# Kernel tuning notes

Measured on AMD Instinct MI355X. Metric: run time of the kernel, lower is better.

The kernel has to match this reference:

```python
import jax, jax.numpy as jnp
import numpy as np

H, W = 72, 128            # raster_h, raster_w
THICK = 0.03              # raster_thickness
SHARP = 80.0              # sigmoid sharpness
RESAMPLE_N = 96           # resample count used for geometric matching costs
PTS_W, TAN_W, CURV_W, OVL_W = 5.0, 1.0, 0.5, 2.0


def _safe_norm(x, axis=-1):
    # faithful to torch.norm; tiny floor only to keep sqrt grad finite
    return jnp.sqrt(jnp.maximum((x * x).sum(axis), 1e-12))


def _grid_xy(h, w):
    ys = jnp.linspace(0.0, 1.0, h)
    xs = jnp.linspace(0.0, 1.0, w)
    yy, xx = jnp.meshgrid(ys, xs, indexing='ij')
    return jnp.stack([xx, yy], axis=-1).reshape(-1, 2)  # [H*W, 2]


def _prepare_mask(vis):
    # mirrors _batched_prepare_curves: fallback to all-ones when <2 visible pts
    raw = vis > 0.5
    fallback = raw.sum(-1) < 2
    return jnp.where(fallback[:, None], 1.0, raw.astype(vis.dtype))  # [m,p]


def _soft_mask(points, point_mask, grid):
    # points [m,p,2], grid [HW,2] -> sigmoid distance field [m, HW]
    seg_a = points[:, :-1]
    ab = points[:, 1:] - seg_a                              # [m,S,2]
    denom = jnp.maximum((ab * ab).sum(-1), 1e-8)            # [m,S]
    seg_valid = (point_mask[:, :-1] * point_mask[:, 1:]) > 0.5
    pts = grid[None, :, None, :]                            # [1,HW,1,2]
    ap = pts - seg_a[:, None]                               # [m,HW,S,2]
    t = jnp.clip((ap * ab[:, None]).sum(-1) / denom[:, None], 0.0, 1.0)
    proj = seg_a[:, None] + t[..., None] * ab[:, None]      # [m,HW,S,2]
    dist = _safe_norm(pts - proj)                           # [m,HW,S]
    dist = jnp.where(seg_valid[:, None, :], dist, jnp.inf)
    min_dist = dist.min(-1)                                 # [m,HW]
    # fallback: curves with no valid segment use nearest visible point
    pdist = _safe_norm(grid[None, :, None, :] - points[:, None])  # [m,HW,p]
    pdist = jnp.where(point_mask[:, None, :] > 0.5, pdist, jnp.inf)
    no_seg = ~seg_valid.any(-1)
    min_dist = jnp.where(no_seg[:, None], pdist.min(-1), min_dist)
    return jax.nn.sigmoid((THICK - min_dist) * SHARP)       # [m,HW]


def _resample(points, point_mask, num):
    # arclength resampling, mirrors _batched_resample_polyline
    m, p, _ = points.shape
    seg_valid = point_mask[:, :-1] * point_mask[:, 1:]
    seg_len = _safe_norm(points[:, 1:] - points[:, :-1]) * seg_valid  # [m,p-1]
    cum = jnp.concatenate([jnp.zeros((m, 1), points.dtype),
                           jnp.cumsum(seg_len, -1)], axis=-1)          # [m,p]
    total = cum[:, -1]
    base_t = jnp.linspace(0.0, 1.0, num)
    t = base_t[None, :] * total[:, None]                               # [m,num]
    idx = jax.vmap(lambda c, tt: jnp.searchsorted(c, tt, side='right'))(cum, t) - 1
    idx = jnp.clip(idx, 0, p - 2)
    left = jnp.take_along_axis(points[:, :-1], idx[..., None], axis=1)
    right = jnp.take_along_axis(points[:, 1:], idx[..., None], axis=1)
    lt = jnp.take_along_axis(cum[:, :-1], idx, axis=1)
    rt = jnp.take_along_axis(cum[:, 1:], idx, axis=1)
    alpha = ((t - lt) / jnp.maximum(rt - lt, 1e-8))[..., None]
    out = left + alpha * (right - left)
    return jnp.where((total < 1e-8)[:, None, None], points[:, :1, :], out)


def _pt2poly(A, B):
    # A [qa,r,2] sample points; B [qb,r,2] polylines -> mean min dist [qa,qb]
    seg_a = B[:, :-1]
    ab = B[:, 1:] - seg_a                                   # [qb,S,2]
    denom = jnp.maximum((ab * ab).sum(-1), 1e-8)            # [qb,S]
    pts = A[:, None, :, None, :]                            # [qa,1,r,1,2]
    ap = pts - seg_a[None, :, None]                         # [qa,qb,r,S,2]
    t = jnp.clip((ap * ab[None, :, None]).sum(-1) / denom[None, :, None], 0.0, 1.0)
    proj = seg_a[None, :, None] + t[..., None] * ab[None, :, None]
    dist = _safe_norm(pts - proj)                           # [qa,qb,r,S]
    return dist.min(-1).mean(-1)                            # [qa,qb]


def _tangents(pts):
    # central differences, endpoints one-sided, unit-normalized
    fwd = jnp.concatenate([pts[:, 1:2] - pts[:, 0:1],
                           pts[:, 2:] - pts[:, :-2],
                           pts[:, -1:] - pts[:, -2:-1]], axis=1)
    n = jnp.maximum(jnp.sqrt((fwd * fwd).sum(-1, keepdims=True)), 1e-8)
    return fwd / n


def _smooth_l1(x):
    a = jnp.abs(x)
    return jnp.where(a < 1.0, 0.5 * a * a, a - 0.5)


def lane_match_cost(pred_pts, gt_pts, gt_vis):
    grid = _grid_xy(H, W)
    m_pred = jnp.ones(pred_pts.shape[:2], pred_pts.dtype)
    m_gt = _prepare_mask(gt_vis)
    # geometric pairwise costs on resampled curves
    pred_rs = _resample(pred_pts, m_pred, RESAMPLE_N)       # [Q,r,2]
    gt_rs = _resample(gt_pts, m_gt, RESAMPLE_N)             # [G,r,2]
    sym = 0.5 * (_pt2poly(pred_rs, gt_rs) + _pt2poly(gt_rs, pred_rs).T)
    pt = _tangents(pred_rs)
    gt_t = _tangents(gt_rs)
    tan = 1.0 - jnp.abs((pt[:, None] * gt_t[None]).sum(-1)).mean(-1)
    ps = pred_rs[:, 2:] - 2 * pred_rs[:, 1:-1] + pred_rs[:, :-2]
    gs = gt_rs[:, 2:] - 2 * gt_rs[:, 1:-1] + gt_rs[:, :-2]
    curv = _smooth_l1(ps[:, None] - gs[None]).mean((-1, -2))
    # soft raster overlap (1 - soft IoU)
    pm = _soft_mask(pred_pts, m_pred, grid)                 # [Q,HW]
    gm = _soft_mask(gt_pts, m_gt, grid)                     # [G,HW]
    inter = pm @ gm.T
    union = pm.sum(-1)[:, None] + gm.sum(-1)[None, :] - inter
    overlap = 1.0 - inter / jnp.maximum(union, 1e-8)
    return PTS_W * sym + TAN_W * tan + CURV_W * curv + OVL_W * overlap


def setup_inputs() -> dict:
    key = jax.random.key(0)
    k1, k2, k3 = jax.random.split(key, 3)
    Q, G, P = 100, 50, 24
    pred_pts = jax.random.uniform(k1, (Q, P, 2), dtype=jnp.float32)
    gt_pts = jax.random.uniform(k2, (G, P, 2), dtype=jnp.float32)
    gt_vis = jax.random.uniform(k3, (G, P), dtype=jnp.float32)
    return {"pred_pts": pred_pts, "gt_pts": gt_pts, "gt_vis": gt_vis}


def reference(pred_pts, gt_pts, gt_vis):
    return lane_match_cost(pred_pts, gt_pts, gt_vis)  # [Q,G] match cost
```

## Files before the change

### kernel.cpp

```cpp
#include <hip/hip_runtime.h>
#include <hip/hip_bf16.h>
#include <math.h>

#define Q_N 100
#define G_N 50
#define P_N 24
#define RS_N 96
#define GRID_N 9216
#define THICK 0.03f
#define SHARP 80.0f
#define PTS_W 5.0f
#define TAN_W 1.0f
#define CURV_W 0.5f
#define OVL_W 2.0f

#define PRS_OFF  0
#define GRS_OFF  19200
#define PMB_OFF  28800
#define GMB_OFF  544896
#define ROWP_OFF 839808
#define ROWG_OFF 840708
#define INTP_OFF 841216

typedef float    f32x2 __attribute__((ext_vector_type(2)));
typedef float    f32x4 __attribute__((ext_vector_type(4)));
typedef _Float16 f16x8 __attribute__((ext_vector_type(8)));

__device__ __forceinline__ float smooth_l1(float x) {
    float a = fabsf(x);
    return (a < 1.0f) ? 0.5f * a * a : a - 0.5f;
}
__device__ __forceinline__ float fast_rcp(float x) {
#if __has_builtin(__builtin_amdgcn_rcpf)
    return __builtin_amdgcn_rcpf(x);
#else
    return 1.0f / x;
#endif
}
__device__ __forceinline__ float fast_sqrt(float x) {
#if __has_builtin(__builtin_amdgcn_sqrtf)
    return __builtin_amdgcn_sqrtf(x);
#else
    return sqrtf(x);
#endif
}

__global__ __launch_bounds__(256)
void mask_kernel(const float* __restrict__ pred,
                 const float* __restrict__ gt,
                 const float* __restrict__ vis,
                 float* __restrict__ ws) {
    int row   = blockIdx.x / 9;
    int chunk = blockIdx.x % 9;
    int tid = threadIdx.x;
    bool isPred = row < Q_N;
    __shared__ float ptx[P_N], pty[P_N], pvv[P_N];
    __shared__ float4 seg[P_N-1];
    __shared__ float  sinv[P_N-1];
    __shared__ int s_noseg;
    __shared__ float wsum[4];
    __shared__ float cum[P_N];
    __shared__ float s_total;

    if (tid < P_N) {
        const float* src = isPred ? pred + row * (P_N*2) : gt + (row - Q_N) * (P_N*2);
        float2 p = ((const float2*)src)[tid];
        ptx[tid] = p.x; pty[tid] = p.y;
    }
    if (tid == 0) {
        s_noseg = 1;
        if (isPred) {
            for (int k = 0; k < P_N; k++) pvv[k] = 1.0f;
        } else {
            const float* v = vis + (row - Q_N) * P_N;
            int cnt = 0;
            for (int k = 0; k < P_N; k++) {
                int r = (v[k] > 0.5f) ? 1 : 0;
                cnt += r;
                pvv[k] = (float)r;
            }
            if (cnt < 2) for (int k = 0; k < P_N; k++) pvv[k] = 1.0f;
        }
    }
    __syncthreads();
    if (tid < P_N-1) {
        bool v = pvv[tid] * pvv[tid+1] > 0.5f;
        if (v) {
            float ax = ptx[tid], ay = pty[tid];
            float abx = ptx[tid+1]-ax, aby = pty[tid+1]-ay;
            seg[tid] = make_float4(ax, ay, abx, aby);
            sinv[tid] = fast_rcp(fmaxf(abx*abx + aby*aby, 1e-8f));
            s_noseg = 0;
        } else {
            seg[tid] = make_float4(1e18f, 1e18f, 0.0f, 0.0f);
            sinv[tid] = 0.0f;
        }
    }
    __syncthreads();

    int g0 = chunk * 1024 + tid * 4;
    float y  = (float)(g0 >> 7) * (1.0f/71.0f);
    float x0 = (float)(g0 & 127) * (1.0f/127.0f);
    f32x2 xs01 = { x0,                  x0 + 1.0f/127.0f };
    f32x2 xs23 = { x0 + 2.0f/127.0f,    x0 + 3.0f/127.0f };
    f32x2 m01 = {3.0e38f, 3.0e38f}, m23 = {3.0e38f, 3.0e38f};
    #pragma unroll
    for (int k = 0; k < P_N-1; k++) {
        float4 sg = seg[k];
        float inv = sinv[k];
        float apy = y - sg.y;
        float dwy = apy * sg.w;
        f32x2 apx01 = xs01 - sg.x;
        f32x2 apx23 = xs23 - sg.x;
        f32x2 t01 = (apx01*sg.z + dwy) * inv;
        f32x2 t23 = (apx23*sg.z + dwy) * inv;
        t01.x = fminf(fmaxf(t01.x, 0.0f), 1.0f);
        t01.y = fminf(fmaxf(t01.y, 0.0f), 1.0f);
        t23.x = fminf(fmaxf(t23.x, 0.0f), 1.0f);
        t23.y = fminf(fmaxf(t23.y, 0.0f), 1.0f);
        f32x2 dx01 = apx01 - t01*sg.z;
        f32x2 dy01 = apy   - t01*sg.w;
        f32x2 dx23 = apx23 - t23*sg.z;
        f32x2 dy23 = apy   - t23*sg.w;
        f32x2 d01 = dx01*dx01 + dy01*dy01;
        f32x2 d23 = dx23*dx23 + dy23*dy23;
        m01.x = fminf(m01.x, d01.x); m01.y = fminf(m01.y, d01.y);
        m23.x = fminf(m23.x, d23.x); m23.y = fminf(m23.y, d23.y);
    }
    float m2[4] = { m01.x, m01.y, m23.x, m23.y };
    if (s_noseg) {
        float xs[4] = { xs01.x, xs01.y, xs23.x, xs23.y };
        #pragma unroll
        for (int u = 0; u < 4; u++) m2[u] = 3.0e38f;
        for (int k = 0; k < P_N; k++) {
            if (pvv[k] > 0.5f) {
                #pragma unroll
                for (int u = 0; u < 4; u++) {
                    float dx = xs[u] - ptx[k], dy = y - pty[k];
                    m2[u] = fminf(m2[u], dx*dx + dy*dy);
                }
            }
        }
    }
    ushort4 o;
    unsigned short* ov = &o.x;
    float lsum = 0.0f;
    #pragma unroll
    for (int u = 0; u < 4; u++) {
        float mind = fast_sqrt(fmaxf(m2[u], 1e-12f));
        float z = (THICK - mind) * SHARP;
        float s = fast_rcp(1.0f + __expf(-z));
        _Float16 h = (_Float16)s;
        ov[u] = __builtin_bit_cast(unsigned short, h);
        lsum += (float)h;
    }
    unsigned short* base = (unsigned short*)(ws + (isPred ? PMB_OFF : GMB_OFF))
                         + (size_t)(isPred ? row : row - Q_N) * GRID_N;
    ((ushort4*)base)[g0 >> 2] = o;

    #pragma unroll
    for (int off = 32; off > 0; off >>= 1) lsum += __shfl_down(lsum, off);
    if ((tid & 63) == 0) wsum[tid >> 6] = lsum;
    __syncthreads();
    if (tid == 0) {
        float s = (wsum[0] + wsum[1]) + (wsum[2] + wsum[3]);
        if (isPred) ws[ROWP_OFF + row*9 + chunk] = s;
        else        ws[ROWG_OFF + (row - Q_N)*9 + chunk] = s;
    }

    if (chunk == 0) {
        if (tid == 0) {
            float c = 0.0f;
            cum[0] = 0.0f;
            for (int k = 0; k < P_N-1; k++) {
                float dx = ptx[k+1]-ptx[k], dy = pty[k+1]-pty[k];
                float len = sqrtf(fmaxf(dx*dx + dy*dy, 1e-12f));
                float valid = pvv[k]*pvv[k+1];
                c += len * valid;
                cum[k+1] = c;
            }
            s_total = c;
        }
        __syncthreads();
        float total = s_total;
        if (tid < RS_N) {
            float ox, oy;
            if (total < 1e-8f) {
                ox = ptx[0]; oy = pty[0];
            } else {
                float t = ((float)tid / 95.0f) * total;
                int idx = -1;
                for (int k = 0; k < P_N; k++) idx += (cum[k] <= t) ? 1 : 0;
                idx = min(max(idx, 0), P_N-2);
                float lt = cum[idx], rt = cum[idx+1];
                float alpha = (t - lt) / fmaxf(rt - lt, 1e-8f);
                ox = ptx[idx] + alpha * (ptx[idx+1]-ptx[idx]);
                oy = pty[idx] + alpha * (pty[idx+1]-pty[idx]);
            }
            float* dst = isPred ? ws + PRS_OFF + row * (RS_N*2)
                                : ws + GRS_OFF + (row - Q_N) * (RS_N*2);
            dst[2*tid]   = ox;
            dst[2*tid+1] = oy;
        }
    }
}

__global__ __launch_bounds__(64)
void inter_kernel(float* __restrict__ ws) {
    int bid = blockIdx.x;
    int mt = bid % 7;
    int nt = (bid / 7) & 3;
    int kc = bid / 28;
    int l = threadIdx.x;
    const unsigned short* PMB = (const unsigned short*)(ws + PMB_OFF);
    const unsigned short* GMB = (const unsigned short*)(ws + GMB_OFF);
    int i0 = mt*16, j0 = nt*16, k0 = kc*1024;
    const f16x8* pa = (const f16x8*)(PMB + (size_t)(i0 + (l & 15)) * GRID_N + k0 + 8*(l >> 4));
    const f16x8* pb = (const f16x8*)(GMB + (size_t)(j0 + (l & 15)) * GRID_N + k0 + 8*(l >> 4));
    f32x4 acc = {0.0f, 0.0f, 0.0f, 0.0f};
    #pragma unroll 8
    for (int s = 0; s < 32; s++) {
        acc = __builtin_amdgcn_mfma_f32_16x16x32_f16(pa[s*4], pb[s*4], acc, 0, 0, 0);
    }
    float* dst = ws + INTP_OFF + kc * 7168;
    int r0 = 4*(l >> 4), c = l & 15;
    #pragma unroll
    for (int v = 0; v < 4; v++) {
        dst[(i0 + r0 + v) * 64 + (j0 + c)] = acc[v];
    }
}

__global__ __launch_bounds__(256)
void pair_kernel(const float* __restrict__ ws, float* __restrict__ out) {
    int bi = blockIdx.x / 25;
    int bj = blockIdx.x % 25;
    int i0 = bi*2, j0 = bj*2;
    int tid = threadIdx.x;
    int w = tid >> 6;
    int l = tid & 63;
    int wi = w >> 1, wj = w & 1;
    int i = i0 + wi, j = j0 + wj;

    __shared__ float Apts[2][RS_N*2], Bpts[2][RS_N*2];
    __shared__ float4 Aseg[2][RS_N-1], Bseg[2][RS_N-1];
    __shared__ float  AInv[2][RS_N-1], BInv[2][RS_N-1];

    float e_ip = 0.0f, e_rp = 0.0f, e_rg = 0.0f;
    if (l < 9) {
        e_ip = ws[INTP_OFF + l*7168 + i*64 + j];
        e_rp = ws[ROWP_OFF + i*9 + l];
        e_rg = ws[ROWG_OFF + j*9 + l];
    }

    if (tid < 192) {
        int side = tid / 96;
        int r = (tid / 48) & 1;
        int o = tid % 48;
        const float4* src = (const float4*)(ws + (side ? GRS_OFF + (j0+r)*(RS_N*2)
                                                       : PRS_OFF + (i0+r)*(RS_N*2)));
        ((float4*)(side ? Bpts[r] : Apts[r]))[o] = src[o];
    }
    __syncthreads();
    for (int q = tid; q < 4*(RS_N-1); q += 256) {
        int side = q / (2*(RS_N-1));
        int rr = (q / (RS_N-1)) & 1;
        int s = q % (RS_N-1);
        const float* P = side ? Bpts[rr] : Apts[rr];
        float ax = P[2*s], ay = P[2*s+1];
        float abx = P[2*s+2]-ax, aby = P[2*s+3]-ay;
        float inv = fast_rcp(fmaxf(abx*abx + aby*aby, 1e-8f));
        if (side) { Bseg[rr][s] = make_float4(ax,ay,abx,aby); BInv[rr][s] = inv; }
        else      { Aseg[rr][s] = make_float4(ax,ay,abx,aby); AInv[rr][s] = inv; }
    }
    __syncthreads();

    bool bSide = l >= 32;
    int h = l & 31;
    const float*  myP = bSide ? Bpts[wj] : Apts[wi];
    const float4* SG  = bSide ? Aseg[wi] : Bseg[wj];
    const float*  SI  = bSide ? AInv[wi] : BInv[wj];
    f32x2 px01 = { myP[6*h+0], myP[6*h+2] };
    f32x2 py01 = { myP[6*h+1], myP[6*h+3] };
    float px2 = myP[6*h+4], py2 = myP[6*h+5];
    f32x2 m01 = {3.0e38f, 3.0e38f};
    float m22 = 3.0e38f;
    #pragma unroll 5
    for (int s = 0; s < RS_N-1; s++) {
        float4 sg = SG[s];
        float inv = SI[s];
        {
            f32x2 apx = px01 - sg.x;
            f32x2 apy = py01 - sg.y;
            f32x2 t = (apx*sg.z + apy*sg.w) * inv;
            t.x = fminf(fmaxf(t.x, 0.0f), 1.0f);
            t.y = fminf(fmaxf(t.y, 0.0f), 1.0f);
            f32x2 dx = apx - t*sg.z;
            f32x2 dy = apy - t*sg.w;
            f32x2 d2 = dx*dx + dy*dy;
            m01.x = fminf(m01.x, d2.x);
            m01.y = fminf(m01.y, d2.y);
        }
        {
            float apx = px2-sg.x, apy = py2-sg.y;
            float t = fminf(fmaxf((apx*sg.z + apy*sg.w)*inv, 0.0f), 1.0f);
            float dx = apx - t*sg.z, dy = apy - t*sg.w;
            m22 = fminf(m22, dx*dx + dy*dy);
        }
    }
    float cham = fast_sqrt(fmaxf(m01.x, 1e-12f)) + fast_sqrt(fmaxf(m01.y, 1e-12f))
               + fast_sqrt(fmaxf(m22, 1e-12f));

    const float* AX = Apts[wi];
    const float* BX = Bpts[wj];
    float tsum = 0.0f, csum = 0.0f;
    #pragma unroll
    for (int rep = 0; rep < 2; rep++) {
        int p = l + rep*64;
        if (p < RS_N) {
            int pl = (p == 0) ? 0 : p-1;
            int pr = (p == RS_N-1) ? RS_N-1 : p+1;
            float tax = AX[2*pr]-AX[2*pl], tay = AX[2*pr+1]-AX[2*pl+1];
            float na = fmaxf(fast_sqrt(tax*tax + tay*tay), 1e-8f);
            float tbx = BX[2*pr]-BX[2*pl], tby = BX[2*pr+1]-BX[2*pl+1];
            float nb = fmaxf(fast_sqrt(tbx*tbx + tby*tby), 1e-8f);
            tsum += fabsf((tax*tbx + tay*tby) * fast_rcp(na*nb));
            if (p < RS_N-2) {
                float psx = AX[2*p+4] - 2.0f*AX[2*p+2] + AX[2*p];
                float psy = AX[2*p+5] - 2.0f*AX[2*p+3] + AX[2*p+1];
                float gsx = BX[2*p+4] - 2.0f*BX[2*p+2] + BX[2*p];
                float gsy = BX[2*p+5] - 2.0f*BX[2*p+3] + BX[2*p+1];
                csum += smooth_l1(psx - gsx) + smooth_l1(psy - gsy);
            }
        }
    }

    #pragma unroll
    for (int off = 32; off > 0; off >>= 1) {
        cham += __shfl_down(cham, off);
        tsum += __shfl_down(tsum, off);
        csum += __shfl_down(csum, off);
    }
    #pragma unroll
    for (int off = 8; off > 0; off >>= 1) {
        e_ip += __shfl_down(e_ip, off);
        e_rp += __shfl_down(e_rp, off);
        e_rg += __shfl_down(e_rg, off);
    }

    if (l == 0) {
        float sym  = cham * (1.0f/192.0f);
        float tanv = 1.0f - tsum * (1.0f/96.0f);
        float cuv  = csum * (1.0f/188.0f);
        float uni  = e_rp + e_rg - e_ip;
        float ovl  = 1.0f - e_ip / fmaxf(uni, 1e-8f);
        out[i * G_N + j] = PTS_W * sym + TAN_W * tanv + CURV_W * cuv + OVL_W * ovl;
    }
}

extern "C" void kernel_launch(void* const* d_in, const int* in_sizes, int n_in,
                              void* d_out, int out_size, void* d_ws, size_t ws_size,
                              hipStream_t stream) {
    (void)in_sizes; (void)n_in; (void)out_size; (void)ws_size;
    const float* pred = (const float*)d_in[0];
    const float* gt   = (const float*)d_in[1];
    const float* vis  = (const float*)d_in[2];
    float* out = (float*)d_out;
    float* ws  = (float*)d_ws;

    mask_kernel<<<(Q_N + G_N) * 9, 256, 0, stream>>>(pred, gt, vis, ws);
    inter_kernel<<<7 * 4 * 9, 64, 0, stream>>>(ws);
    pair_kernel<<<50 * 25, 256, 0, stream>>>(ws, out);
}
```

Before: 46.53 us.

## Process 4x2 pair tile per block with 16-lane chamfer groups

Each pair_kernel block now handles 4 pred × 2 gt curves (8 pairs) instead of 2×2, halving the grid and loading 6 curves into shared memory per block. The chamfer work is split so each 16-thread group handles one direction of one pair, with 6 points per thread. Segment inverse lengths are recomputed in the inner loop rather than stored. Partial sums go through shared memory and a final sync. This amortizes curve loads and segment setup across more pairs, at the cost of extra per-iteration rcp work and more work per thread.

```diff
diff --git a/kernel.cpp b/kernel.cpp
--- a/kernel.cpp
+++ b/kernel.cpp
@@ -234,123 +234,117 @@
 void pair_kernel(const float* __restrict__ ws, float* __restrict__ out) {
     int bi = blockIdx.x / 25;
     int bj = blockIdx.x % 25;
-    int i0 = bi*2, j0 = bj*2;
+    int i0 = bi*4, j0 = bj*2;
     int tid = threadIdx.x;
-    int w = tid >> 6;
-    int l = tid & 63;
-    int wi = w >> 1, wj = w & 1;
-    int i = i0 + wi, j = j0 + wj;
-
-    __shared__ float Apts[2][RS_N*2], Bpts[2][RS_N*2];
-    __shared__ float4 Aseg[2][RS_N-1], Bseg[2][RS_N-1];
-    __shared__ float  AInv[2][RS_N-1], BInv[2][RS_N-1];
+
+    __shared__ float Apts[4][RS_N*2], Bpts[2][RS_N*2];
+    __shared__ float4 Aseg[4][RS_N-1], Bseg[2][RS_N-1];
+    __shared__ float chamLds[16], tanLds[8], curvLds[8];
 
     float e_ip = 0.0f, e_rp = 0.0f, e_rg = 0.0f;
-    if (l < 9) {
-        e_ip = ws[INTP_OFF + l*7168 + i*64 + j];
-        e_rp = ws[ROWP_OFF + i*9 + l];
-        e_rg = ws[ROWG_OFF + j*9 + l];
-    }
-
-    if (tid < 192) {
-        int side = tid / 96;
-        int r = (tid / 48) & 1;
-        int o = tid % 48;
-        const float4* src = (const float4*)(ws + (side ? GRS_OFF + (j0+r)*(RS_N*2)
-                                                       : PRS_OFF + (i0+r)*(RS_N*2)));
-        ((float4*)(side ? Bpts[r] : Apts[r]))[o] = src[o];
-    }
-    __syncthreads();
-    for (int q = tid; q < 4*(RS_N-1); q += 256) {
-        int side = q / (2*(RS_N-1));
-        int rr = (q / (RS_N-1)) & 1;
-        int s = q % (RS_N-1);
-        const float* P = side ? Bpts[rr] : Apts[rr];
+    if (tid < 8) {
+        int i = i0 + (tid >> 1), j = j0 + (tid & 1);
+        #pragma unroll
+        for (int k = 0; k < 9; k++) {
+            e_ip += ws[INTP_OFF + k*7168 + i*64 + j];
+            e_rp += ws[ROWP_OFF + i*9 + k];
+            e_rg += ws[ROWG_OFF + j*9 + k];
+        }
+    }
+
+    for (int q2 = tid; q2 < 288; q2 += 256) {
+        int row = q2 / 48, o = q2 % 48;
+        if (row < 4) ((float4*)Apts[row])[o]   = ((const float4*)(ws + PRS_OFF + (size_t)(i0+row)*(RS_N*2)))[o];
+        else         ((float4*)Bpts[row-4])[o] = ((const float4*)(ws + GRS_OFF + (size_t)(j0+row-4)*(RS_N*2)))[o];
+    }
+    __syncthreads();
+    for (int q2 = tid; q2 < 6*(RS_N-1); q2 += 256) {
+        int row = q2 / (RS_N-1), s = q2 % (RS_N-1);
+        const float* P = (row < 4) ? Apts[row] : Bpts[row-4];
         float ax = P[2*s], ay = P[2*s+1];
-        float abx = P[2*s+2]-ax, aby = P[2*s+3]-ay;
-        float inv = fast_rcp(fmaxf(abx*abx + aby*aby, 1e-8f));
-        if (side) { Bseg[rr][s] = make_float4(ax,ay,abx,aby); BInv[rr][s] = inv; }
-        else      { Aseg[rr][s] = make_float4(ax,ay,abx,aby); AInv[rr][s] = inv; }
-    }
-    __syncthreads();
-
-    bool bSide = l >= 32;
-    int h = l & 31;
-    const float*  myP = bSide ? Bpts[wj] : Apts[wi];
-    const float4* SG  = bSide ? Aseg[wi] : Bseg[wj];
-    const float*  SI  = bSide ? AInv[wi] : BInv[wj];
-    f32x2 px01 = { myP[6*h+0], myP[6*h+2] };
-    f32x2 py01 = { myP[6*h+1], myP[6*h+3] };
-    float px2 = myP[6*h+4], py2 = myP[6*h+5];
-    f32x2 m01 = {3.0e38f, 3.0e38f};
-    float m22 = 3.0e38f;
-    #pragma unroll 5
-    for (int s = 0; s < RS_N-1; s++) {
-        float4 sg = SG[s];
-        float inv = SI[s];
-        {
-            f32x2 apx = px01 - sg.x;
-            f32x2 apy = py01 - sg.y;
-            f32x2 t = (apx*sg.z + apy*sg.w) * inv;
-            t.x = fminf(fmaxf(t.x, 0.0f), 1.0f);
-            t.y = fminf(fmaxf(t.y, 0.0f), 1.0f);
-            f32x2 dx = apx - t*sg.z;
-            f32x2 dy = apy - t*sg.w;
-            f32x2 d2 = dx*dx + dy*dy;
-            m01.x = fminf(m01.x, d2.x);
-            m01.y = fminf(m01.y, d2.y);
-        }
-        {
-            float apx = px2-sg.x, apy = py2-sg.y;
-            float t = fminf(fmaxf((apx*sg.z + apy*sg.w)*inv, 0.0f), 1.0f);
-            float dx = apx - t*sg.z, dy = apy - t*sg.w;
-            m22 = fminf(m22, dx*dx + dy*dy);
-        }
-    }
-    float cham = fast_sqrt(fmaxf(m01.x, 1e-12f)) + fast_sqrt(fmaxf(m01.y, 1e-12f))
-               + fast_sqrt(fmaxf(m22, 1e-12f));
-
-    const float* AX = Apts[wi];
-    const float* BX = Bpts[wj];
-    float tsum = 0.0f, csum = 0.0f;
-    #pragma unroll
-    for (int rep = 0; rep < 2; rep++) {
-        int p = l + rep*64;
-        if (p < RS_N) {
-            int pl = (p == 0) ? 0 : p-1;
-            int pr = (p == RS_N-1) ? RS_N-1 : p+1;
+        float4 v = make_float4(ax, ay, P[2*s+2]-ax, P[2*s+3]-ay);
+        if (row < 4) Aseg[row][s] = v; else Bseg[row-4][s] = v;
+    }
+    __syncthreads();
+
+    {
+        int g = tid >> 4, q = tid & 15;
+        int dir = g >> 3, idx = g & 7, r = idx >> 1, c = idx & 1;
+        const float*  P  = dir ? Bpts[c] : Apts[r];
+        const float4* SG = dir ? Aseg[r] : Bseg[c];
+        f32x2 px[3], py[3];
+        #pragma unroll
+        for (int u = 0; u < 3; u++) {
+            px[u] = (f32x2){ P[12*q + 4*u + 0], P[12*q + 4*u + 2] };
+            py[u] = (f32x2){ P[12*q + 4*u + 1], P[12*q + 4*u + 3] };
+        }
+        f32x2 mm[3] = {{3.0e38f,3.0e38f},{3.0e38f,3.0e38f},{3.0e38f,3.0e38f}};
+        #pragma unroll 5
+        for (int s = 0; s < RS_N-1; s++) {
+            float4 sg = SG[s];
+            float inv = fast_rcp(fmaxf(sg.z*sg.z + sg.w*sg.w, 1e-8f));
+            #pragma unroll
+            for (int u = 0; u < 3; u++) {
+                f32x2 apx = px[u] - sg.x;
+                f32x2 apy = py[u] - sg.y;
+                f32x2 t = (apx*sg.z + apy*sg.w) * inv;
+                t.x = fminf(fmaxf(t.x, 0.0f), 1.0f);
+                t.y = fminf(fmaxf(t.y, 0.0f), 1.0f);
+                f32x2 dx = apx - t*sg.z;
+                f32x2 dy = apy - t*sg.w;
+                f32x2 d2 = dx*dx + dy*dy;
+                mm[u].x = fminf(mm[u].x, d2.x);
+                mm[u].y = fminf(mm[u].y, d2.y);
+            }
+        }
+        float cham = 0.0f;
+        #pragma unroll
+        for (int u = 0; u < 3; u++) {
+            cham += fast_sqrt(fmaxf(mm[u].x, 1e-12f)) + fast_sqrt(fmaxf(mm[u].y, 1e-12f));
+        }
+        #pragma unroll
+        for (int off = 8; off > 0; off >>= 1) cham += __shfl_down(cham, off);
+        if (q == 0) chamLds[g] = cham;
+    }
+
+    {
+        int p = tid >> 5, q32 = tid & 31;
+        const float* AX = Apts[p >> 1];
+        const float* BX = Bpts[p & 1];
+        float tsum = 0.0f, csum = 0.0f;
+        #pragma unroll
+        for (int rep = 0; rep < 3; rep++) {
+            int pt = q32 + rep*32;
+            int pl = (pt == 0) ? 0 : pt-1;
+            int pr = (pt == RS_N-1) ? RS_N-1 : pt+1;
             float tax = AX[2*pr]-AX[2*pl], tay = AX[2*pr+1]-AX[2*pl+1];
             float na = fmaxf(fast_sqrt(tax*tax + tay*tay), 1e-8f);
             float tbx = BX[2*pr]-BX[2*pl], tby = BX[2*pr+1]-BX[2*pl+1];
             float nb = fmaxf(fast_sqrt(tbx*tbx + tby*tby), 1e-8f);
             tsum += fabsf((tax*tbx + tay*tby) * fast_rcp(na*nb));
-            if (p < RS_N-2) {
-                float psx = AX[2*p+4] - 2.0f*AX[2*p+2] + AX[2*p];
-                float psy = AX[2*p+5] - 2.0f*AX[2*p+3] + AX[2*p+1];
-                float gsx = BX[2*p+4] - 2.0f*BX[2*p+2] + BX[2*p];
-                float gsy = BX[2*p+5] - 2.0f*BX[2*p+3] + BX[2*p+1];
+            if (pt < RS_N-2) {
+                float psx = AX[2*pt+4] - 2.0f*AX[2*pt+2] + AX[2*pt];
+                float psy = AX[2*pt+5] - 2.0f*AX[2*pt+3] + AX[2*pt+1];
+                float gsx = BX[2*pt+4] - 2.0f*BX[2*pt+2] + BX[2*pt];
+                float gsy = BX[2*pt+5] - 2.0f*BX[2*pt+3] + BX[2*pt+1];
                 csum += smooth_l1(psx - gsx) + smooth_l1(psy - gsy);
             }
         }
-    }
-
-    #pragma unroll
-    for (int off = 32; off > 0; off >>= 1) {
-        cham += __shfl_down(cham, off);
-        tsum += __shfl_down(tsum, off);
-        csum += __shfl_down(csum, off);
-    }
-    #pragma unroll
-    for (int off = 8; off > 0; off >>= 1) {
-        e_ip += __shfl_down(e_ip, off);
-        e_rp += __shfl_down(e_rp, off);
-        e_rg += __shfl_down(e_rg, off);
-    }
-
-    if (l == 0) {
-        float sym  = cham * (1.0f/192.0f);
-        float tanv = 1.0f - tsum * (1.0f/96.0f);
-        float cuv  = csum * (1.0f/188.0f);
+        #pragma unroll
+        for (int off = 16; off > 0; off >>= 1) {
+            tsum += __shfl_down(tsum, off);
+            csum += __shfl_down(csum, off);
+        }
+        if (q32 == 0) { tanLds[p] = tsum; curvLds[p] = csum; }
+    }
+    __syncthreads();
+
+    if (tid < 8) {
+        int p = tid;
+        int i = i0 + (p >> 1), j = j0 + (p & 1);
+        float sym  = (chamLds[p] + chamLds[8+p]) * (1.0f/192.0f);
+        float tanv = 1.0f - tanLds[p] * (1.0f/96.0f);
+        float cuv  = curvLds[p] * (1.0f/188.0f);
         float uni  = e_rp + e_rg - e_ip;
         float ovl  = 1.0f - e_ip / fmaxf(uni, 1e-8f);
         out[i * G_N + j] = PTS_W * sym + TAN_W * tanv + CURV_W * cuv + OVL_W * ovl;
@@ -369,5 +363,5 @@
 
     mask_kernel<<<(Q_N + G_N) * 9, 256, 0, stream>>>(pred, gt, vis, ws);
     inter_kernel<<<7 * 4 * 9, 64, 0, stream>>>(ws);
-    pair_kernel<<<50 * 25, 256, 0, stream>>>(ws, out);
-}
+    pair_kernel<<<25 * 25, 256, 0, stream>>>(ws, out);
+}
```

New measurement: 50.48 us. 8.5% more time.

## Precompute segment tables in mask kernel and broadcast segments via readlane

Applied to the files above, without the earlier changes.

The mask kernel now writes per-row segment origins, directions and inverse squared lengths to workspace, so the pair kernel no longer rebuilds them in shared memory each block. In the pair kernel each wave loads one row's segments into registers and broadcasts them with readlane while evaluating chamfer distances. The work split across waves is reorganised so each wave handles one segment row against two point sets, with partial sums combined through shared memory. This removes one barrier and the LDS segment reads, at the cost of extra global writes and reads and a cross-wave reduction.

```diff
diff --git a/kernel.cpp b/kernel.cpp
--- a/kernel.cpp
+++ b/kernel.cpp
@@ -21,6 +21,8 @@
 #define ROWP_OFF 839808
 #define ROWG_OFF 840708
 #define INTP_OFF 841216
+#define SEGT_OFF 905728
+#define INVT_OFF 962728
 
 typedef float    f32x2 __attribute__((ext_vector_type(2)));
 typedef float    f32x4 __attribute__((ext_vector_type(4)));
@@ -42,6 +44,13 @@
     return __builtin_amdgcn_sqrtf(x);
 #else
     return sqrtf(x);
+#endif
+}
+__device__ __forceinline__ float rlf(float v, int s) {
+#if __has_builtin(__builtin_amdgcn_readlane)
+    return __builtin_bit_cast(float, __builtin_amdgcn_readlane(__builtin_bit_cast(int, v), s));
+#else
+    return __shfl(v, s);
 #endif
 }
 
@@ -61,6 +70,7 @@
     __shared__ float wsum[4];
     __shared__ float cum[P_N];
     __shared__ float s_total;
+    __shared__ float rpx[RS_N], rpy[RS_N];
 
     if (tid < P_N) {
         const float* src = isPred ? pred + row * (P_N*2) : gt + (row - Q_N) * (P_N*2);
@@ -197,10 +207,17 @@
                 ox = ptx[idx] + alpha * (ptx[idx+1]-ptx[idx]);
                 oy = pty[idx] + alpha * (pty[idx+1]-pty[idx]);
             }
+            rpx[tid] = ox; rpy[tid] = oy;
             float* dst = isPred ? ws + PRS_OFF + row * (RS_N*2)
                                 : ws + GRS_OFF + (row - Q_N) * (RS_N*2);
             dst[2*tid]   = ox;
             dst[2*tid+1] = oy;
+        }
+        __syncthreads();
+        if (tid < RS_N-1) {
+            float abx = rpx[tid+1]-rpx[tid], aby = rpy[tid+1]-rpy[tid];
+            ((float4*)(ws + SEGT_OFF))[row*95 + tid] = make_float4(rpx[tid], rpy[tid], abx, aby);
+            ws[INVT_OFF + row*95 + tid] = fast_rcp(fmaxf(abx*abx + aby*aby, 1e-8f));
         }
     }
 }
@@ -242,8 +259,7 @@
     int i = i0 + wi, j = j0 + wj;
 
     __shared__ float Apts[2][RS_N*2], Bpts[2][RS_N*2];
-    __shared__ float4 Aseg[2][RS_N-1], Bseg[2][RS_N-1];
-    __shared__ float  AInv[2][RS_N-1], BInv[2][RS_N-1];
+    __shared__ float chamLds[4][2];
 
     float e_ip = 0.0f, e_rp = 0.0f, e_rg = 0.0f;
     if (l < 9) {
@@ -260,55 +276,64 @@
                                                        : PRS_OFF + (i0+r)*(RS_N*2)));
         ((float4*)(side ? Bpts[r] : Apts[r]))[o] = src[o];
     }
-    __syncthreads();
-    for (int q = tid; q < 4*(RS_N-1); q += 256) {
-        int side = q / (2*(RS_N-1));
-        int rr = (q / (RS_N-1)) & 1;
-        int s = q % (RS_N-1);
-        const float* P = side ? Bpts[rr] : Apts[rr];
-        float ax = P[2*s], ay = P[2*s+1];
-        float abx = P[2*s+2]-ax, aby = P[2*s+3]-ay;
-        float inv = fast_rcp(fmaxf(abx*abx + aby*aby, 1e-8f));
-        if (side) { Bseg[rr][s] = make_float4(ax,ay,abx,aby); BInv[rr][s] = inv; }
-        else      { Aseg[rr][s] = make_float4(ax,ay,abx,aby); AInv[rr][s] = inv; }
-    }
-    __syncthreads();
-
-    bool bSide = l >= 32;
-    int h = l & 31;
-    const float*  myP = bSide ? Bpts[wj] : Apts[wi];
-    const float4* SG  = bSide ? Aseg[wi] : Bseg[wj];
-    const float*  SI  = bSide ? AInv[wi] : BInv[wj];
-    f32x2 px01 = { myP[6*h+0], myP[6*h+2] };
-    f32x2 py01 = { myP[6*h+1], myP[6*h+3] };
-    float px2 = myP[6*h+4], py2 = myP[6*h+5];
+
+    int segRow = (w < 2) ? (100 + j0 + w) : (i0 + (w - 2));
+    const float4* st = (const float4*)(ws + SEGT_OFF) + segRow*95;
+    const float*  it = ws + INVT_OFF + segRow*95;
+    float4 sA = st[l];
+    float  ivA = it[l];
+    float4 sB = (l < 31) ? st[64 + l] : make_float4(0.0f, 0.0f, 0.0f, 0.0f);
+    float  ivB = (l < 31) ? it[64 + l] : 0.0f;
+
+    __syncthreads();
+
+    int q = l & 31;
+    const float* P = (w < 2) ? Apts[l >> 5] : Bpts[l >> 5];
+    f32x2 px01 = { P[6*q+0], P[6*q+2] };
+    f32x2 py01 = { P[6*q+1], P[6*q+3] };
+    float px2 = P[6*q+4], py2 = P[6*q+5];
     f32x2 m01 = {3.0e38f, 3.0e38f};
     float m22 = 3.0e38f;
-    #pragma unroll 5
-    for (int s = 0; s < RS_N-1; s++) {
-        float4 sg = SG[s];
-        float inv = SI[s];
-        {
-            f32x2 apx = px01 - sg.x;
-            f32x2 apy = py01 - sg.y;
-            f32x2 t = (apx*sg.z + apy*sg.w) * inv;
-            t.x = fminf(fmaxf(t.x, 0.0f), 1.0f);
-            t.y = fminf(fmaxf(t.y, 0.0f), 1.0f);
-            f32x2 dx = apx - t*sg.z;
-            f32x2 dy = apy - t*sg.w;
-            f32x2 d2 = dx*dx + dy*dy;
-            m01.x = fminf(m01.x, d2.x);
-            m01.y = fminf(m01.y, d2.y);
-        }
-        {
-            float apx = px2-sg.x, apy = py2-sg.y;
-            float t = fminf(fmaxf((apx*sg.z + apy*sg.w)*inv, 0.0f), 1.0f);
-            float dx = apx - t*sg.z, dy = apy - t*sg.w;
-            m22 = fminf(m22, dx*dx + dy*dy);
-        }
-    }
+
+#define CHAM_EVAL(AX, AY, BX, BY, IV)                                          \
+    {                                                                          \
+        f32x2 apx = px01 - (AX);                                               \
+        f32x2 apy = py01 - (AY);                                               \
+        f32x2 t = (apx*(BX) + apy*(BY)) * (IV);                                \
+        t.x = fminf(fmaxf(t.x, 0.0f), 1.0f);                                   \
+        t.y = fminf(fmaxf(t.y, 0.0f), 1.0f);                                   \
+        f32x2 dx = apx - t*(BX);                                               \
+        f32x2 dy = apy - t*(BY);                                               \
+        f32x2 d2 = dx*dx + dy*dy;                                              \
+        m01.x = fminf(m01.x, d2.x);                                            \
+        m01.y = fminf(m01.y, d2.y);                                            \
+        float apx2 = px2 - (AX), apy2 = py2 - (AY);                            \
+        float t2 = fminf(fmaxf((apx2*(BX) + apy2*(BY))*(IV), 0.0f), 1.0f);     \
+        float dx2 = apx2 - t2*(BX), dy2 = apy2 - t2*(BY);                      \
+        m22 = fminf(m22, dx2*dx2 + dy2*dy2);                                   \
+    }
+
+    #pragma unroll 8
+    for (int s = 0; s < 64; s++) {
+        float ax = rlf(sA.x, s), ay = rlf(sA.y, s);
+        float bx = rlf(sA.z, s), by = rlf(sA.w, s);
+        float iv = rlf(ivA, s);
+        CHAM_EVAL(ax, ay, bx, by, iv)
+    }
+    #pragma unroll 8
+    for (int s = 0; s < 31; s++) {
+        float ax = rlf(sB.x, s), ay = rlf(sB.y, s);
+        float bx = rlf(sB.z, s), by = rlf(sB.w, s);
+        float iv = rlf(ivB, s);
+        CHAM_EVAL(ax, ay, bx, by, iv)
+    }
+#undef CHAM_EVAL
+
     float cham = fast_sqrt(fmaxf(m01.x, 1e-12f)) + fast_sqrt(fmaxf(m01.y, 1e-12f))
                + fast_sqrt(fmaxf(m22, 1e-12f));
+    #pragma unroll
+    for (int off = 16; off > 0; off >>= 1) cham += __shfl_down(cham, off, 32);
+    if ((l & 31) == 0) chamLds[w][l >> 5] = cham;
 
     const float* AX = Apts[wi];
     const float* BX = Bpts[wj];
@@ -333,10 +358,8 @@
             }
         }
     }
-
     #pragma unroll
     for (int off = 32; off > 0; off >>= 1) {
-        cham += __shfl_down(cham, off);
         tsum += __shfl_down(tsum, off);
         csum += __shfl_down(csum, off);
     }
@@ -346,9 +369,10 @@
         e_rp += __shfl_down(e_rp, off);
         e_rg += __shfl_down(e_rg, off);
     }
+    __syncthreads();
 
     if (l == 0) {
-        float sym  = cham * (1.0f/192.0f);
+        float sym  = (chamLds[wj][wi] + chamLds[2+wi][wj]) * (1.0f/192.0f);
         float tanv = 1.0f - tsum * (1.0f/96.0f);
         float cuv  = csum * (1.0f/188.0f);
         float uni  = e_rp + e_rg - e_ip;
```

New measurement: 51.86 us. 11.5% more time.

## Fuse mask intersection dot products into pair kernel, drop separate MFMA GEMM kernel

Applied to the files above, without the earlier changes.

Removes the standalone inter_kernel that computed pred×gt mask intersections as a tiled f16 MFMA GEMM with split-K partials. Each wave in pair_kernel now computes its own (i,j) dot product over the 9216-element masks using MFMA on 16 chunks, taking the diagonal entries of the result and reducing them with shuffles. This saves a kernel launch and the partial-sum round trip through global memory. In exchange, every wave reads its full pred and gt mask rows again, which means far more global and L2 traffic than the tiled GEMM, and only the diagonal of each MFMA result is used. The workspace offsets were also repacked.

```diff
diff --git a/kernel.cpp b/kernel.cpp
--- a/kernel.cpp
+++ b/kernel.cpp
@@ -17,10 +17,9 @@
 #define PRS_OFF  0
 #define GRS_OFF  19200
 #define PMB_OFF  28800
-#define GMB_OFF  544896
-#define ROWP_OFF 839808
-#define ROWG_OFF 840708
-#define INTP_OFF 841216
+#define GMB_OFF  489600
+#define ROWP_OFF 720000
+#define ROWG_OFF 720900
 
 typedef float    f32x2 __attribute__((ext_vector_type(2)));
 typedef float    f32x4 __attribute__((ext_vector_type(4)));
@@ -205,31 +204,6 @@
     }
 }
 
-__global__ __launch_bounds__(64)
-void inter_kernel(float* __restrict__ ws) {
-    int bid = blockIdx.x;
-    int mt = bid % 7;
-    int nt = (bid / 7) & 3;
-    int kc = bid / 28;
-    int l = threadIdx.x;
-    const unsigned short* PMB = (const unsigned short*)(ws + PMB_OFF);
-    const unsigned short* GMB = (const unsigned short*)(ws + GMB_OFF);
-    int i0 = mt*16, j0 = nt*16, k0 = kc*1024;
-    const f16x8* pa = (const f16x8*)(PMB + (size_t)(i0 + (l & 15)) * GRID_N + k0 + 8*(l >> 4));
-    const f16x8* pb = (const f16x8*)(GMB + (size_t)(j0 + (l & 15)) * GRID_N + k0 + 8*(l >> 4));
-    f32x4 acc = {0.0f, 0.0f, 0.0f, 0.0f};
-    #pragma unroll 8
-    for (int s = 0; s < 32; s++) {
-        acc = __builtin_amdgcn_mfma_f32_16x16x32_f16(pa[s*4], pb[s*4], acc, 0, 0, 0);
-    }
-    float* dst = ws + INTP_OFF + kc * 7168;
-    int r0 = 4*(l >> 4), c = l & 15;
-    #pragma unroll
-    for (int v = 0; v < 4; v++) {
-        dst[(i0 + r0 + v) * 64 + (j0 + c)] = acc[v];
-    }
-}
-
 __global__ __launch_bounds__(256)
 void pair_kernel(const float* __restrict__ ws, float* __restrict__ out) {
     int bi = blockIdx.x / 25;
@@ -245,11 +219,26 @@
     __shared__ float4 Aseg[2][RS_N-1], Bseg[2][RS_N-1];
     __shared__ float  AInv[2][RS_N-1], BInv[2][RS_N-1];
 
-    float e_ip = 0.0f, e_rp = 0.0f, e_rg = 0.0f;
+    float e_rp = 0.0f, e_rg = 0.0f;
     if (l < 9) {
-        e_ip = ws[INTP_OFF + l*7168 + i*64 + j];
         e_rp = ws[ROWP_OFF + i*9 + l];
         e_rg = ws[ROWG_OFF + j*9 + l];
+    }
+
+    const f16x8* pa = (const f16x8*)((const unsigned short*)(ws + PMB_OFF) + (size_t)i * GRID_N)
+                    + (l & 15)*4 + (l >> 4);
+    const f16x8* pb = (const f16x8*)((const unsigned short*)(ws + GMB_OFF) + (size_t)j * GRID_N)
+                    + (l & 15)*4 + (l >> 4);
+    f32x4 acc = {0.0f, 0.0f, 0.0f, 0.0f};
+    #pragma unroll 6
+    for (int c = 0; c < 18; c++) {
+        acc = __builtin_amdgcn_mfma_f32_16x16x32_f16(pa[c*64], pb[c*64], acc, 0, 0, 0);
+    }
+    float dot = 0.0f;
+    {
+        int r0 = 4*(l >> 4), cc = l & 15;
+        #pragma unroll
+        for (int v = 0; v < 4; v++) dot = (cc == r0 + v) ? acc[v] : dot;
     }
 
     if (tid < 192) {
@@ -339,10 +328,10 @@
         cham += __shfl_down(cham, off);
         tsum += __shfl_down(tsum, off);
         csum += __shfl_down(csum, off);
+        dot  += __shfl_down(dot,  off);
     }
     #pragma unroll
     for (int off = 8; off > 0; off >>= 1) {
-        e_ip += __shfl_down(e_ip, off);
         e_rp += __shfl_down(e_rp, off);
         e_rg += __shfl_down(e_rg, off);
     }
@@ -351,8 +340,8 @@
         float sym  = cham * (1.0f/192.0f);
         float tanv = 1.0f - tsum * (1.0f/96.0f);
         float cuv  = csum * (1.0f/188.0f);
-        float uni  = e_rp + e_rg - e_ip;
-        float ovl  = 1.0f - e_ip / fmaxf(uni, 1e-8f);
+        float uni  = e_rp + e_rg - dot;
+        float ovl  = 1.0f - dot / fmaxf(uni, 1e-8f);
         out[i * G_N + j] = PTS_W * sym + TAN_W * tanv + CURV_W * cuv + OVL_W * ovl;
     }
 }
@@ -368,6 +357,5 @@
     float* ws  = (float*)d_ws;
 
     mask_kernel<<<(Q_N + G_N) * 9, 256, 0, stream>>>(pred, gt, vis, ws);
-    inter_kernel<<<7 * 4 * 9, 64, 0, stream>>>(ws);
     pair_kernel<<<50 * 25, 256, 0, stream>>>(ws, out);
 }
```

Measured after the change: 49.29 us. 1.06x slower.
